# Kernel tuning notes

Hardware: AMD Instinct MI355X
Metric: run time of the kernel (lower is better)

Reference implementation:

```python
import jax, jax.numpy as jnp
import numpy as np

N_NODES = 100000
K_HOPS = 10
ALPHA = 0.1


def gcn_conv(x, src, dst, W, b, num_nodes):
    # GCNConv: linear first (cheaper: out_dim small), then D^-1/2 (A+I) D^-1/2 aggregation
    h = x @ W  # [N, out]
    deg = jax.ops.segment_sum(jnp.ones_like(dst, dtype=h.dtype), dst, num_segments=num_nodes)
    dinv = jnp.where(deg > 0, jax.lax.rsqrt(deg), 0.0)
    norm = dinv[src] * dinv[dst]  # [E]
    msg = h[src] * norm[:, None]
    out = jax.ops.segment_sum(msg, dst, num_segments=num_nodes)
    return out + b


def _with_self_loops(edge_index, num_nodes):
    loops = jnp.arange(num_nodes, dtype=edge_index.dtype)
    src = jnp.concatenate([edge_index[0], loops])
    dst = jnp.concatenate([edge_index[1], loops])
    return src, dst


def setup_inputs() -> dict:
    key = jax.random.key(0)
    ks = jax.random.split(key, 8)
    n_feat, hidden, n_cls, n_edges = 512, 16, 7, 3200000
    x = jax.random.normal(ks[0], (N_NODES, n_feat), dtype=jnp.float32)
    edge_index = jax.random.randint(ks[1], (2, n_edges), 0, N_NODES, dtype=jnp.int64)
    W1 = jax.random.normal(ks[2], (n_feat, hidden), dtype=jnp.float32) * 0.05
    b1 = jnp.zeros((hidden,), dtype=jnp.float32)
    Wl = jax.random.normal(ks[3], (hidden, hidden), dtype=jnp.float32) * 0.25
    bl = jnp.zeros((hidden,), dtype=jnp.float32)
    W2 = jax.random.normal(ks[4], (hidden, n_cls), dtype=jnp.float32) * 0.25
    b2 = jnp.zeros((n_cls,), dtype=jnp.float32)
    return {"x": x, "edge_index": edge_index, "W1": W1, "b1": b1, "Wl": Wl, "bl": bl, "W2": W2, "b2": b2}


def reference(x, edge_index, W1, b1, Wl, bl, W2, b2):
    src, dst = _with_self_loops(edge_index, N_NODES)
    h = jax.nn.relu(gcn_conv(x, src, dst, W1, b1, N_NODES))
    def body(h, _):
        h = ALPHA * jax.nn.relu(h @ Wl + bl) + (1.0 - ALPHA) * h
        return h, None
    h, _ = jax.lax.scan(body, h, None, length=K_HOPS)
    out = gcn_conv(h, src, dst, W2, b2, N_NODES)
    return jax.nn.log_softmax(out, axis=1)
```

## Files before the change

### kernel.cpp

```cpp
#include <hip/hip_runtime.h>
#include <math.h>

#define N_NODES 100000
#define N_EDGES 3200000
#define F_IN    512
#define HID     16
#define NCLS    7
#define ALPHA   0.1f
#define K_HOPS  10

#define SHIFT   7
#define BWIDTH  128
#define NBUCK   ((N_NODES + BWIDTH - 1) / BWIDTH)
#define CHUNK   4096
#define BIN_T   512
#define EPT     (CHUNK / BIN_T)
#define A3_BLOCKS ((N_EDGES + CHUNK - 1) / CHUNK)

#define OFF_BCNT    0u
#define OFF_BSTART  1024u
#define OFF_BCUR    2048u
#define OFF_RP      3072u
#define OFF_DINV    103424u
#define OFF_COL     203776u
#define OFF_BINNED  3403776u
#define OFF_H0      6603776u
#define OFF_H1      8203776u
#define OFF_Z       9803776u

__global__ void k_bhist(const int* __restrict__ dst, int* __restrict__ bcnt) {
    __shared__ int h[NBUCK];
    int tid = threadIdx.x;
    for (int i = tid; i < NBUCK; i += 256) h[i] = 0;
    __syncthreads();
    for (int e = blockIdx.x * 256 + tid; e < N_EDGES; e += gridDim.x * 256)
        atomicAdd(&h[dst[e] >> SHIFT], 1);
    __syncthreads();
    for (int i = tid; i < NBUCK; i += 256) {
        int v = h[i];
        if (v) atomicAdd(&bcnt[i], v);
    }
}

__global__ void k_bscan(const int* __restrict__ bcnt, int* __restrict__ bstart,
                        int* __restrict__ bcur) {
    __shared__ int s[1024];
    int tid = threadIdx.x;
    int v = (tid < NBUCK) ? bcnt[tid] : 0;
    s[tid] = v;
    __syncthreads();
    for (int off = 1; off < 1024; off <<= 1) {
        int t = (tid >= off) ? s[tid - off] : 0;
        __syncthreads();
        s[tid] += t;
        __syncthreads();
    }
    if (tid < NBUCK) {
        int ex = s[tid] - v;
        bstart[tid] = ex;
        bcur[tid] = ex;
    }
    if (tid == 0) bstart[NBUCK] = N_EDGES;
}

__global__ void __launch_bounds__(BIN_T)
k_bin(const int* __restrict__ src, const int* __restrict__ dst,
      int* __restrict__ bcur, unsigned int* __restrict__ binned) {
    __shared__ int ha[NBUCK];
    __shared__ int gbase[NBUCK];
    __shared__ int lcur[NBUCK];
    int tid = threadIdx.x;
    int e0 = blockIdx.x * CHUNK;
    int e1 = e0 + CHUNK;
    if (e1 > N_EDGES) e1 = N_EDGES;
    for (int i = tid; i < NBUCK; i += BIN_T) ha[i] = 0;
    __syncthreads();
    int dloc[EPT];
#pragma unroll
    for (int i = 0; i < EPT; i++) {
        int e = e0 + tid + i * BIN_T;
        dloc[i] = (e < e1) ? dst[e] : -1;
        if (dloc[i] >= 0) atomicAdd(&ha[dloc[i] >> SHIFT], 1);
    }
    __syncthreads();
    for (int s = tid; s < NBUCK; s += BIN_T) {
        int c = ha[s];
        lcur[s] = 0;
        gbase[s] = c ? atomicAdd(&bcur[s], c) : 0;
    }
    __syncthreads();
#pragma unroll
    for (int i = 0; i < EPT; i++) {
        int d = dloc[i];
        if (d >= 0) {
            int e = e0 + tid + i * BIN_T;
            int bk = d >> SHIFT;
            int idx = atomicAdd(&lcur[bk], 1);
            binned[gbase[bk] + idx] =
                ((unsigned int)(d & (BWIDTH - 1)) << 17) | (unsigned int)src[e];
        }
    }
}

__global__ void __launch_bounds__(512)
k_csr(const unsigned int* __restrict__ binned, const int* __restrict__ bstart,
      int* __restrict__ rp, float* __restrict__ dinv, int* __restrict__ col) {
    __shared__ int cnt[BWIDTH];
    __shared__ int s[BWIDTH];
    __shared__ int cur[BWIDTH];
    int tid = threadIdx.x;
    int b = blockIdx.x;
    int base = b << SHIFT;
    int e0 = bstart[b], e1 = bstart[b + 1];
    if (tid < BWIDTH) cnt[tid] = 0;
    __syncthreads();
    for (int e = e0 + tid; e < e1; e += 512)
        atomicAdd(&cnt[binned[e] >> 17], 1);
    __syncthreads();
    int v = 0;
    if (tid < BWIDTH) { v = cnt[tid]; s[tid] = v; }
    __syncthreads();
    for (int off = 1; off < BWIDTH; off <<= 1) {
        int t = 0;
        if (tid < BWIDTH && tid >= off) t = s[tid - off];
        __syncthreads();
        if (tid < BWIDTH) s[tid] += t;
        __syncthreads();
    }
    if (tid < BWIDTH) {
        int ex = s[tid] - v;
        cur[tid] = ex;
        int node = base + tid;
        if (node < N_NODES) {
            rp[node] = e0 + ex;
            dinv[node] = rsqrtf((float)(v + 1));
        }
    }
    if (b == 0 && tid == 0) rp[N_NODES] = N_EDGES;
    __syncthreads();
    for (int e = e0 + tid; e < e1; e += 512) {
        unsigned int w = binned[e];
        int ln = (int)(w >> 17);
        int p = atomicAdd(&cur[ln], 1);
        col[e0 + p] = (int)(w & 0x1FFFFu);
    }
}

#define XWN_BLOCKS 512
#define XWN_WAVES  (XWN_BLOCKS * 4)

__device__ __forceinline__ float4 shfl4_xor(float4 v, int m) {
    float4 r;
    r.x = __shfl_xor(v.x, m);
    r.y = __shfl_xor(v.y, m);
    r.z = __shfl_xor(v.z, m);
    r.w = __shfl_xor(v.w, m);
    return r;
}
__device__ __forceinline__ float4 add4(float4 a, float4 b) {
    a.x += b.x; a.y += b.y; a.z += b.z; a.w += b.w;
    return a;
}

__global__ void __launch_bounds__(256)
k_xw1(const float* __restrict__ x, const float* __restrict__ W,
      const float* __restrict__ dinv, float* __restrict__ h0s) {
    int lane = threadIdx.x & 63;
    int wid = (blockIdx.x * 256 + threadIdx.x) >> 6;

    float4 w[32];
    const float4* W4 = (const float4*)W;
#pragma unroll
    for (int j = 0; j < 8; j++) {
#pragma unroll
        for (int q = 0; q < 4; q++)
            w[j * 4 + q] = W4[(8 * lane + j) * 4 + q];
    }

    int node = wid;
    const float4* xr0 = (const float4*)(x + (size_t)node * F_IN) + 2 * lane;
    float4 xc0 = xr0[0];
    float4 xc1 = xr0[1];

    for (; node < N_NODES; node += XWN_WAVES) {
        int nn = node + XWN_WAVES;
        float4 xn0, xn1;
        if (nn < N_NODES) {
            const float4* xr = (const float4*)(x + (size_t)nn * F_IN) + 2 * lane;
            xn0 = xr[0];
            xn1 = xr[1];
        }

        float xa0 = xc0.x, xa1 = xc0.y, xa2 = xc0.z, xa3 = xc0.w;
        float xa4 = xc1.x, xa5 = xc1.y, xa6 = xc1.z, xa7 = xc1.w;

        float4 pp0 = make_float4(0.f, 0.f, 0.f, 0.f);
        float4 pp1 = pp0, pp2 = pp0, pp3 = pp0;
#define XW_FMA(J, XA)                                            \
        pp0.x += XA * w[J*4+0].x; pp0.y += XA * w[J*4+0].y;      \
        pp0.z += XA * w[J*4+0].z; pp0.w += XA * w[J*4+0].w;      \
        pp1.x += XA * w[J*4+1].x; pp1.y += XA * w[J*4+1].y;      \
        pp1.z += XA * w[J*4+1].z; pp1.w += XA * w[J*4+1].w;      \
        pp2.x += XA * w[J*4+2].x; pp2.y += XA * w[J*4+2].y;      \
        pp2.z += XA * w[J*4+2].z; pp2.w += XA * w[J*4+2].w;      \
        pp3.x += XA * w[J*4+3].x; pp3.y += XA * w[J*4+3].y;      \
        pp3.z += XA * w[J*4+3].z; pp3.w += XA * w[J*4+3].w;
        XW_FMA(0, xa0) XW_FMA(1, xa1) XW_FMA(2, xa2) XW_FMA(3, xa3)
        XW_FMA(4, xa4) XW_FMA(5, xa5) XW_FMA(6, xa6) XW_FMA(7, xa7)
#undef XW_FMA

        int b5 = (lane >> 5) & 1;
        float4 k0 = b5 ? pp2 : pp0;
        float4 k1 = b5 ? pp3 : pp1;
        float4 s0 = b5 ? pp0 : pp2;
        float4 s1 = b5 ? pp1 : pp3;
        k0 = add4(k0, shfl4_xor(s0, 32));
        k1 = add4(k1, shfl4_xor(s1, 32));

        int b4 = (lane >> 4) & 1;
        float4 kk = b4 ? k1 : k0;
        float4 ss = b4 ? k0 : k1;
        kk = add4(kk, shfl4_xor(ss, 16));

        int b3 = (lane >> 3) & 1;
        float e0 = b3 ? kk.z : kk.x;
        float e1 = b3 ? kk.w : kk.y;
        float f0 = b3 ? kk.x : kk.z;
        float f1 = b3 ? kk.y : kk.w;
        e0 += __shfl_xor(f0, 8);
        e1 += __shfl_xor(f1, 8);

        int b2 = (lane >> 2) & 1;
        float v = b2 ? e1 : e0;
        float sv = b2 ? e0 : e1;
        v += __shfl_xor(sv, 4);

        v += __shfl_xor(v, 1);
        v += __shfl_xor(v, 2);

        if ((lane & 3) == 0) {
            float dv = dinv[node];
            h0s[(size_t)node * HID + (lane >> 2)] = dv * v;
        }

        xc0 = xn0;
        xc1 = xn1;
    }
}

__global__ void k_agg1(const float* __restrict__ h0s, const int* __restrict__ rp,
                       const int* __restrict__ col, const float* __restrict__ dinv,
                       const float* __restrict__ b1, float* __restrict__ h1) {
    int node = (blockIdx.x * blockDim.x + threadIdx.x) >> 6;
    if (node >= N_NODES) return;
    int lane = threadIdx.x & 63;
    int c = lane & 15, eo = lane >> 4;
    int e0 = rp[node], e1 = rp[node + 1];
    float acc = 0.f;
    int e = e0 + eo;
    for (; e + 12 < e1; e += 16) {
        int c0 = col[e];
        int c1 = col[e + 4];
        int c2 = col[e + 8];
        int c3 = col[e + 12];
        float v0 = h0s[(size_t)c0 * HID + c];
        float v1 = h0s[(size_t)c1 * HID + c];
        float v2 = h0s[(size_t)c2 * HID + c];
        float v3 = h0s[(size_t)c3 * HID + c];
        acc += v0;
        acc += v1;
        acc += v2;
        acc += v3;
    }
    for (; e + 4 < e1; e += 8) {
        int c0 = col[e];
        int c1 = col[e + 4];
        float v0 = h0s[(size_t)c0 * HID + c];
        float v1 = h0s[(size_t)c1 * HID + c];
        acc += v0;
        acc += v1;
    }
    if (e < e1) acc += h0s[(size_t)col[e] * HID + c];
    acc += __shfl_xor(acc, 16);
    acc += __shfl_xor(acc, 32);
    float o = dinv[node] * (acc + h0s[(size_t)node * HID + c]) + b1[c];
    if (eo == 0) h1[(size_t)node * HID + c] = fmaxf(o, 0.f);
}

__global__ void k_hops(const float* __restrict__ h1, const float* __restrict__ Wl,
                       const float* __restrict__ bl, const float* __restrict__ W2,
                       const float* __restrict__ dinv, float* __restrict__ zs) {
    int node = blockIdx.x * blockDim.x + threadIdx.x;
    if (node >= N_NODES) return;
    float h[HID];
    const float4* h4 = (const float4*)(h1 + (size_t)node * HID);
#pragma unroll
    for (int q = 0; q < HID / 4; q++) {
        float4 v = h4[q];
        h[q * 4 + 0] = v.x; h[q * 4 + 1] = v.y;
        h[q * 4 + 2] = v.z; h[q * 4 + 3] = v.w;
    }
    for (int it = 0; it < K_HOPS; it++) {
        float tm[HID];
#pragma unroll
        for (int c = 0; c < HID; c++) tm[c] = bl[c];
#pragma unroll
        for (int k = 0; k < HID; k++) {
            float hk = h[k];
#pragma unroll
            for (int c = 0; c < HID; c++) tm[c] += hk * Wl[k * HID + c];
        }
#pragma unroll
        for (int c = 0; c < HID; c++)
            h[c] = ALPHA * fmaxf(tm[c], 0.f) + (1.f - ALPHA) * h[c];
    }
    float dv = dinv[node];
    float zz[8];
#pragma unroll
    for (int c = 0; c < 8; c++) zz[c] = 0.f;
#pragma unroll
    for (int k = 0; k < HID; k++) {
        float hk = h[k];
#pragma unroll
        for (int c = 0; c < NCLS; c++) zz[c] += hk * W2[k * NCLS + c];
    }
    float4* z4 = (float4*)(zs + (size_t)node * 8);
    float4 v0, v1;
    v0.x = dv * zz[0]; v0.y = dv * zz[1]; v0.z = dv * zz[2]; v0.w = dv * zz[3];
    v1.x = dv * zz[4]; v1.y = dv * zz[5]; v1.z = dv * zz[6]; v1.w = 0.f;
    z4[0] = v0; z4[1] = v1;
}

__global__ void k_agg2(const float* __restrict__ zs, const int* __restrict__ rp,
                       const int* __restrict__ col, const float* __restrict__ dinv,
                       const float* __restrict__ b2, float* __restrict__ out) {
    int node = (blockIdx.x * blockDim.x + threadIdx.x) >> 6;
    if (node >= N_NODES) return;
    int lane = threadIdx.x & 63;
    int c = lane & 7, eo = lane >> 3;
    int e0 = rp[node], e1 = rp[node + 1];
    float acc = 0.f;
    int e = e0 + eo;
    for (; e + 24 < e1; e += 32) {
        int c0 = col[e];
        int c1 = col[e + 8];
        int c2 = col[e + 16];
        int c3 = col[e + 24];
        float v0 = zs[(size_t)c0 * 8 + c];
        float v1 = zs[(size_t)c1 * 8 + c];
        float v2 = zs[(size_t)c2 * 8 + c];
        float v3 = zs[(size_t)c3 * 8 + c];
        acc += v0;
        acc += v1;
        acc += v2;
        acc += v3;
    }
    for (; e + 8 < e1; e += 16) {
        int c0 = col[e];
        int c1 = col[e + 8];
        float v0 = zs[(size_t)c0 * 8 + c];
        float v1 = zs[(size_t)c1 * 8 + c];
        acc += v0;
        acc += v1;
    }
    if (e < e1) acc += zs[(size_t)col[e] * 8 + c];
    acc += __shfl_xor(acc, 8);
    acc += __shfl_xor(acc, 16);
    acc += __shfl_xor(acc, 32);
    float o = dinv[node] * (acc + zs[(size_t)node * 8 + c]) + ((c < NCLS) ? b2[c] : 0.f);
    float val = (c < NCLS) ? o : -INFINITY;
    float m = val;
    m = fmaxf(m, __shfl_xor(m, 1));
    m = fmaxf(m, __shfl_xor(m, 2));
    m = fmaxf(m, __shfl_xor(m, 4));
    float ex = (c < NCLS) ? expf(o - m) : 0.f;
    float ss = ex;
    ss += __shfl_xor(ss, 1);
    ss += __shfl_xor(ss, 2);
    ss += __shfl_xor(ss, 4);
    if (eo == 0 && c < NCLS) out[(size_t)node * NCLS + c] = o - m - logf(ss);
}

extern "C" void kernel_launch(void* const* d_in, const int* in_sizes, int n_in,
                              void* d_out, int out_size, void* d_ws, size_t ws_size,
                              hipStream_t stream) {
    const float* x  = (const float*)d_in[0];
    const int*   ei = (const int*)d_in[1];
    const float* W1 = (const float*)d_in[2];
    const float* b1 = (const float*)d_in[3];
    const float* Wl = (const float*)d_in[4];
    const float* bl = (const float*)d_in[5];
    const float* W2 = (const float*)d_in[6];
    const float* b2 = (const float*)d_in[7];
    float* out = (float*)d_out;

    int*   wsI = (int*)d_ws;
    float* wsF = (float*)d_ws;
    int*          bcnt   = wsI + OFF_BCNT;
    int*          bstart = wsI + OFF_BSTART;
    int*          bcur   = wsI + OFF_BCUR;
    int*          rp     = wsI + OFF_RP;
    float*        dinv   = wsF + OFF_DINV;
    int*          col    = wsI + OFF_COL;
    unsigned int* binned = (unsigned int*)(wsI + OFF_BINNED);
    float*        h0s    = wsF + OFF_H0;
    float*        h1     = wsF + OFF_H1;
    float*        zs     = wsF + OFF_Z;

    const int* src = ei;
    const int* dst = ei + N_EDGES;

    hipMemsetAsync(bcnt, 0, NBUCK * sizeof(int), stream);

    k_bhist<<<1024, 256, 0, stream>>>(dst, bcnt);
    k_bscan<<<1, 1024, 0, stream>>>(bcnt, bstart, bcur);
    k_bin<<<A3_BLOCKS, BIN_T, 0, stream>>>(src, dst, bcur, binned);
    k_csr<<<NBUCK, 512, 0, stream>>>(binned, bstart, rp, dinv, col);
    k_xw1<<<XWN_BLOCKS, 256, 0, stream>>>(x, W1, dinv, h0s);
    k_agg1<<<(N_NODES * 64 + 255) / 256, 256, 0, stream>>>(h0s, rp, col, dinv, b1, h1);
    k_hops<<<(N_NODES + 255) / 256, 256, 0, stream>>>(h1, Wl, bl, W2, dinv, zs);
    k_agg2<<<(N_NODES * 64 + 255) / 256, 256, 0, stream>>>(zs, rp, col, dinv, b2, out);
}
```

Baseline: 558.1 us.

## Use fixed-size bucket slabs, fuse first aggregation with hop iterations

Drops the bucket histogram and scan kernels. Each destination bucket now gets a fixed SLAB-sized region, and k_csr reads its edge count from the atomic cursor. A per-node degree array replaces rp[node+1]. The first aggregation is fused with the 10 propagation hops and the W2 projection, with the hops done per lane via wave shuffles, which removes the h1 round trip and one launch. k_xw1 now prefetches x rows two iterations ahead. The risk is that a bucket receiving more than SLAB edges would overflow into the next slab; this holds only for roughly uniform destination distributions.

```diff
diff --git a/kernel.cpp b/kernel.cpp
--- a/kernel.cpp
+++ b/kernel.cpp
@@ -12,56 +12,20 @@
 #define SHIFT   7
 #define BWIDTH  128
 #define NBUCK   ((N_NODES + BWIDTH - 1) / BWIDTH)
+#define SLAB    5120
 #define CHUNK   4096
 #define BIN_T   512
 #define EPT     (CHUNK / BIN_T)
 #define A3_BLOCKS ((N_EDGES + CHUNK - 1) / CHUNK)
 
-#define OFF_BCNT    0u
-#define OFF_BSTART  1024u
-#define OFF_BCUR    2048u
-#define OFF_RP      3072u
-#define OFF_DINV    103424u
-#define OFF_COL     203776u
-#define OFF_BINNED  3403776u
-#define OFF_H0      6603776u
-#define OFF_H1      8203776u
-#define OFF_Z       9803776u
-
-__global__ void k_bhist(const int* __restrict__ dst, int* __restrict__ bcnt) {
-    __shared__ int h[NBUCK];
-    int tid = threadIdx.x;
-    for (int i = tid; i < NBUCK; i += 256) h[i] = 0;
-    __syncthreads();
-    for (int e = blockIdx.x * 256 + tid; e < N_EDGES; e += gridDim.x * 256)
-        atomicAdd(&h[dst[e] >> SHIFT], 1);
-    __syncthreads();
-    for (int i = tid; i < NBUCK; i += 256) {
-        int v = h[i];
-        if (v) atomicAdd(&bcnt[i], v);
-    }
-}
-
-__global__ void k_bscan(const int* __restrict__ bcnt, int* __restrict__ bstart,
-                        int* __restrict__ bcur) {
-    __shared__ int s[1024];
-    int tid = threadIdx.x;
-    int v = (tid < NBUCK) ? bcnt[tid] : 0;
-    s[tid] = v;
-    __syncthreads();
-    for (int off = 1; off < 1024; off <<= 1) {
-        int t = (tid >= off) ? s[tid - off] : 0;
-        __syncthreads();
-        s[tid] += t;
-        __syncthreads();
-    }
-    if (tid < NBUCK) {
-        int ex = s[tid] - v;
-        bstart[tid] = ex;
-        bcur[tid] = ex;
-    }
-    if (tid == 0) bstart[NBUCK] = N_EDGES;
-}
+#define OFF_BCUR    0u
+#define OFF_RP      1024u
+#define OFF_DEG     101376u
+#define OFF_DINV    201728u
+#define OFF_COL     302080u
+#define OFF_BINNED  4305920u
+#define OFF_H0      8309760u
+#define OFF_Z       9909760u
 
 __global__ void __launch_bounds__(BIN_T)
 k_bin(const int* __restrict__ src, const int* __restrict__ dst,
@@ -86,7 +50,7 @@
     for (int s = tid; s < NBUCK; s += BIN_T) {
         int c = ha[s];
         lcur[s] = 0;
-        gbase[s] = c ? atomicAdd(&bcur[s], c) : 0;
+        gbase[s] = c ? (s * SLAB + atomicAdd(&bcur[s], c)) : 0;
     }
     __syncthreads();
 #pragma unroll
@@ -103,15 +67,17 @@
 }
 
 __global__ void __launch_bounds__(512)
-k_csr(const unsigned int* __restrict__ binned, const int* __restrict__ bstart,
-      int* __restrict__ rp, float* __restrict__ dinv, int* __restrict__ col) {
+k_csr(const unsigned int* __restrict__ binned, const int* __restrict__ bcur,
+      int* __restrict__ rp, int* __restrict__ deg, float* __restrict__ dinv,
+      int* __restrict__ col) {
     __shared__ int cnt[BWIDTH];
     __shared__ int s[BWIDTH];
     __shared__ int cur[BWIDTH];
     int tid = threadIdx.x;
     int b = blockIdx.x;
     int base = b << SHIFT;
-    int e0 = bstart[b], e1 = bstart[b + 1];
+    int e0 = b * SLAB;
+    int e1 = e0 + bcur[b];
     if (tid < BWIDTH) cnt[tid] = 0;
     __syncthreads();
     for (int e = e0 + tid; e < e1; e += 512)
@@ -133,10 +99,10 @@
         int node = base + tid;
         if (node < N_NODES) {
             rp[node] = e0 + ex;
+            deg[node] = v;
             dinv[node] = rsqrtf((float)(v + 1));
         }
     }
-    if (b == 0 && tid == 0) rp[N_NODES] = N_EDGES;
     __syncthreads();
     for (int e = e0 + tid; e < e1; e += 512) {
         unsigned int w = binned[e];
@@ -178,17 +144,26 @@
     }
 
     int node = wid;
-    const float4* xr0 = (const float4*)(x + (size_t)node * F_IN) + 2 * lane;
-    float4 xc0 = xr0[0];
-    float4 xc1 = xr0[1];
+    float4 xc0, xc1, xn0, xn1;
+    if (node < N_NODES) {
+        const float4* xr = (const float4*)(x + (size_t)node * F_IN) + 2 * lane;
+        xc0 = xr[0];
+        xc1 = xr[1];
+    }
+    int n1 = node + XWN_WAVES;
+    if (n1 < N_NODES) {
+        const float4* xr = (const float4*)(x + (size_t)n1 * F_IN) + 2 * lane;
+        xn0 = xr[0];
+        xn1 = xr[1];
+    }
 
     for (; node < N_NODES; node += XWN_WAVES) {
-        int nn = node + XWN_WAVES;
-        float4 xn0, xn1;
-        if (nn < N_NODES) {
-            const float4* xr = (const float4*)(x + (size_t)nn * F_IN) + 2 * lane;
-            xn0 = xr[0];
-            xn1 = xr[1];
+        int n2 = node + 2 * XWN_WAVES;
+        float4 xp0, xp1;
+        if (n2 < N_NODES) {
+            const float4* xr = (const float4*)(x + (size_t)n2 * F_IN) + 2 * lane;
+            xp0 = xr[0];
+            xp1 = xr[1];
         }
 
         float xa0 = xc0.x, xa1 = xc0.y, xa2 = xc0.z, xa3 = xc0.w;
@@ -243,19 +218,21 @@
             h0s[(size_t)node * HID + (lane >> 2)] = dv * v;
         }
 
-        xc0 = xn0;
-        xc1 = xn1;
-    }
-}
-
-__global__ void k_agg1(const float* __restrict__ h0s, const int* __restrict__ rp,
-                       const int* __restrict__ col, const float* __restrict__ dinv,
-                       const float* __restrict__ b1, float* __restrict__ h1) {
+        xc0 = xn0; xc1 = xn1;
+        xn0 = xp0; xn1 = xp1;
+    }
+}
+
+__global__ void k_agg1hops(const float* __restrict__ h0s, const int* __restrict__ rp,
+                           const int* __restrict__ deg, const int* __restrict__ col,
+                           const float* __restrict__ dinv, const float* __restrict__ b1,
+                           const float* __restrict__ Wl, const float* __restrict__ bl,
+                           const float* __restrict__ W2, float* __restrict__ zs) {
     int node = (blockIdx.x * blockDim.x + threadIdx.x) >> 6;
     if (node >= N_NODES) return;
     int lane = threadIdx.x & 63;
     int c = lane & 15, eo = lane >> 4;
-    int e0 = rp[node], e1 = rp[node + 1];
+    int e0 = rp[node], e1 = e0 + deg[node];
     float acc = 0.f;
     int e = e0 + eo;
     for (; e + 12 < e1; e += 16) {
@@ -283,62 +260,41 @@
     if (e < e1) acc += h0s[(size_t)col[e] * HID + c];
     acc += __shfl_xor(acc, 16);
     acc += __shfl_xor(acc, 32);
-    float o = dinv[node] * (acc + h0s[(size_t)node * HID + c]) + b1[c];
-    if (eo == 0) h1[(size_t)node * HID + c] = fmaxf(o, 0.f);
-}
-
-__global__ void k_hops(const float* __restrict__ h1, const float* __restrict__ Wl,
-                       const float* __restrict__ bl, const float* __restrict__ W2,
-                       const float* __restrict__ dinv, float* __restrict__ zs) {
-    int node = blockIdx.x * blockDim.x + threadIdx.x;
-    if (node >= N_NODES) return;
-    float h[HID];
-    const float4* h4 = (const float4*)(h1 + (size_t)node * HID);
-#pragma unroll
-    for (int q = 0; q < HID / 4; q++) {
-        float4 v = h4[q];
-        h[q * 4 + 0] = v.x; h[q * 4 + 1] = v.y;
-        h[q * 4 + 2] = v.z; h[q * 4 + 3] = v.w;
-    }
+
+    float dv = dinv[node];
+    float o = dv * (acc + h0s[(size_t)node * HID + c]) + b1[c];
+    float h = fmaxf(o, 0.f);
+
+    int bs = lane & 48;
     for (int it = 0; it < K_HOPS; it++) {
-        float tm[HID];
-#pragma unroll
-        for (int c = 0; c < HID; c++) tm[c] = bl[c];
+        float tm = bl[c];
 #pragma unroll
         for (int k = 0; k < HID; k++) {
-            float hk = h[k];
-#pragma unroll
-            for (int c = 0; c < HID; c++) tm[c] += hk * Wl[k * HID + c];
-        }
-#pragma unroll
-        for (int c = 0; c < HID; c++)
-            h[c] = ALPHA * fmaxf(tm[c], 0.f) + (1.f - ALPHA) * h[c];
-    }
-    float dv = dinv[node];
-    float zz[8];
-#pragma unroll
-    for (int c = 0; c < 8; c++) zz[c] = 0.f;
+            float hk = __shfl(h, bs + k);
+            tm += hk * Wl[k * HID + c];
+        }
+        h = ALPHA * fmaxf(tm, 0.f) + (1.f - ALPHA) * h;
+    }
+
+    float zz = 0.f;
 #pragma unroll
     for (int k = 0; k < HID; k++) {
-        float hk = h[k];
-#pragma unroll
-        for (int c = 0; c < NCLS; c++) zz[c] += hk * W2[k * NCLS + c];
-    }
-    float4* z4 = (float4*)(zs + (size_t)node * 8);
-    float4 v0, v1;
-    v0.x = dv * zz[0]; v0.y = dv * zz[1]; v0.z = dv * zz[2]; v0.w = dv * zz[3];
-    v1.x = dv * zz[4]; v1.y = dv * zz[5]; v1.z = dv * zz[6]; v1.w = 0.f;
-    z4[0] = v0; z4[1] = v1;
+        float hk = __shfl(h, bs + k);
+        float w2v = (c < NCLS) ? W2[k * NCLS + c] : 0.f;
+        zz += hk * w2v;
+    }
+    if (eo == 0 && c < 8) zs[(size_t)node * 8 + c] = dv * zz;
 }
 
 __global__ void k_agg2(const float* __restrict__ zs, const int* __restrict__ rp,
-                       const int* __restrict__ col, const float* __restrict__ dinv,
-                       const float* __restrict__ b2, float* __restrict__ out) {
+                       const int* __restrict__ deg, const int* __restrict__ col,
+                       const float* __restrict__ dinv, const float* __restrict__ b2,
+                       float* __restrict__ out) {
     int node = (blockIdx.x * blockDim.x + threadIdx.x) >> 6;
     if (node >= N_NODES) return;
     int lane = threadIdx.x & 63;
     int c = lane & 7, eo = lane >> 3;
-    int e0 = rp[node], e1 = rp[node + 1];
+    int e0 = rp[node], e1 = e0 + deg[node];
     float acc = 0.f;
     int e = e0 + eo;
     for (; e + 24 < e1; e += 32) {
@@ -396,28 +352,24 @@
 
     int*   wsI = (int*)d_ws;
     float* wsF = (float*)d_ws;
-    int*          bcnt   = wsI + OFF_BCNT;
-    int*          bstart = wsI + OFF_BSTART;
     int*          bcur   = wsI + OFF_BCUR;
     int*          rp     = wsI + OFF_RP;
+    int*          deg    = wsI + OFF_DEG;
     float*        dinv   = wsF + OFF_DINV;
     int*          col    = wsI + OFF_COL;
     unsigned int* binned = (unsigned int*)(wsI + OFF_BINNED);
     float*        h0s    = wsF + OFF_H0;
-    float*        h1     = wsF + OFF_H1;
     float*        zs     = wsF + OFF_Z;
 
     const int* src = ei;
     const int* dst = ei + N_EDGES;
 
-    hipMemsetAsync(bcnt, 0, NBUCK * sizeof(int), stream);
-
-    k_bhist<<<1024, 256, 0, stream>>>(dst, bcnt);
-    k_bscan<<<1, 1024, 0, stream>>>(bcnt, bstart, bcur);
+    hipMemsetAsync(bcur, 0, NBUCK * sizeof(int), stream);
+
     k_bin<<<A3_BLOCKS, BIN_T, 0, stream>>>(src, dst, bcur, binned);
-    k_csr<<<NBUCK, 512, 0, stream>>>(binned, bstart, rp, dinv, col);
+    k_csr<<<NBUCK, 512, 0, stream>>>(binned, bcur, rp, deg, dinv, col);
     k_xw1<<<XWN_BLOCKS, 256, 0, stream>>>(x, W1, dinv, h0s);
-    k_agg1<<<(N_NODES * 64 + 255) / 256, 256, 0, stream>>>(h0s, rp, col, dinv, b1, h1);
-    k_hops<<<(N_NODES + 255) / 256, 256, 0, stream>>>(h1, Wl, bl, W2, dinv, zs);
-    k_agg2<<<(N_NODES * 64 + 255) / 256, 256, 0, stream>>>(zs, rp, col, dinv, b2, out);
-}
+    k_agg1hops<<<(N_NODES * 64 + 255) / 256, 256, 0, stream>>>(h0s, rp, deg, col, dinv,
+                                                               b1, Wl, bl, W2, zs);
+    k_agg2<<<(N_NODES * 64 + 255) / 256, 256, 0, stream>>>(zs, rp, deg, col, dinv, b2, out);
+}
```

Result: slower. 644.3 us (+15.5%).
